# Kernel optimization log

Measured on AMD Instinct MI355X. Metric: run time of the kernel, lower is better.

Reference implementation:

```python
import jax, jax.numpy as jnp
import numpy as np

N_NODES = 50000
N_EDGES = 800000
D_IN = 128
HID = 128
N_CLS = 5
BN_EPS = 1e-5


def setup_inputs() -> dict:
    key = jax.random.key(0)
    ks = jax.random.split(key, 8)

    def lin(k, fan_in, shape):
        return (jax.random.normal(k, shape, jnp.float32) / np.sqrt(fan_in)).astype(jnp.float32)

    inp = {
        'x': jax.random.normal(ks[0], (N_NODES, D_IN), jnp.float32),
        'edge_index': jax.random.randint(ks[1], (2, N_EDGES), 0, N_NODES, dtype=jnp.int64),
        'W0': lin(ks[2], D_IN, (D_IN, HID)), 'b0': jnp.zeros((HID,), jnp.float32),
        'g0': jnp.ones((HID,), jnp.float32), 'be0': jnp.zeros((HID,), jnp.float32),
        'W1': lin(ks[3], HID, (HID, HID)), 'b1': jnp.zeros((HID,), jnp.float32),
        'g1': jnp.ones((HID,), jnp.float32), 'be1': jnp.zeros((HID,), jnp.float32),
        'W2': lin(ks[4], HID, (HID, HID)), 'b2': jnp.zeros((HID,), jnp.float32),
        'g2': jnp.ones((HID,), jnp.float32), 'be2': jnp.zeros((HID,), jnp.float32),
        'cW1': lin(ks[5], HID, (HID, HID // 2)), 'cb1': jnp.zeros((HID // 2,), jnp.float32),
        'cW2': lin(ks[6], HID // 2, (HID // 2, N_CLS)), 'cb2': jnp.zeros((N_CLS,), jnp.float32),
    }
    return inp


def _gcn_conv(x, src, dst, W, b):
    # H = D~^{-1/2} (A+I) D~^{-1/2} X W + b  (Kipf & Welling / PyG GCNConv)
    h = x @ W                                           # [N, out]
    deg = jnp.zeros((N_NODES,), h.dtype).at[dst].add(1.0) + 1.0  # degree incl. self-loop
    dinv = jax.lax.rsqrt(deg)                           # D~^{-1/2}
    norm = dinv[src] * dinv[dst]                        # [E]
    agg = jnp.zeros_like(h).at[dst].add(h[src] * norm[:, None])
    agg = agg + h * (dinv * dinv)[:, None]              # self-loop term
    return agg + b


def _batchnorm(x, gamma, beta):
    # training-mode BatchNorm1d over the node dimension
    mean = x.mean(axis=0)
    var = x.var(axis=0)
    return gamma * (x - mean) * jax.lax.rsqrt(var + BN_EPS) + beta


def reference(x, edge_index, W0, b0, g0, be0, W1, b1, g1, be1, W2, b2, g2, be2,
              cW1, cb1, cW2, cb2):
    src, dst = edge_index[0], edge_index[1]
    for W, b, g, be in ((W0, b0, g0, be0), (W1, b1, g1, be1), (W2, b2, g2, be2)):
        x = _gcn_conv(x, src, dst, W, b)
        x = _batchnorm(x, g, be)
        x = jax.nn.relu(x)
        # dropout: identity (eval / deterministic reference)
    pooled = x.mean(axis=0, keepdims=True)              # [1, HID]
    h = jax.nn.relu(pooled @ cW1 + cb1)
    return h @ cW2 + cb2                                # [1, N_CLS]
```

## Files before the change

### kernel.cpp

```cpp
#include <hip/hip_runtime.h>
#include <hip/hip_fp16.h>
#include <cstdint>
#include <cstddef>

#define D 128
#define NAGG 2048
#define SCAN_BLOCKS 256
#define FILL_PASSES 8
#define EPT 4

using f16x4 = __attribute__((ext_vector_type(4))) _Float16;
using f32x4 = __attribute__((ext_vector_type(4))) float;

__device__ __forceinline__ int swz(int row, int byte) {
  return row * 256 + (((byte)&0xF0) ^ ((row & 7) << 4)) + ((byte)&0x0F);
}


__global__ void count_kernel(const int* __restrict__ ei, int* __restrict__ counts, int E) {
  for (int e = blockIdx.x * blockDim.x + threadIdx.x; e < E; e += gridDim.x * blockDim.x) {
    int d = ei[(size_t)E + e];
    atomicAdd(&counts[d], 1);
  }
}

__global__ __launch_bounds__(256) void scan1_kernel(const int* __restrict__ counts,
                                                    int* __restrict__ blocksums, int N) {
  __shared__ int red[256];
  const int b = blockIdx.x, t = threadIdx.x;
  const int chunk = (N + SCAN_BLOCKS - 1) / SCAN_BLOCKS;
  const int lo = b * chunk, hi = min(lo + chunk, N);
  int s = 0;
  for (int i = lo + t; i < hi; i += 256) s += counts[i];
  red[t] = s;
  __syncthreads();
  for (int off = 128; off > 0; off >>= 1) {
    if (t < off) red[t] += red[t + off];
    __syncthreads();
  }
  if (t == 0) blocksums[b] = red[0];
}

__global__ __launch_bounds__(256) void scan2_kernel(int* __restrict__ blocksums) {
  __shared__ int part[256];
  const int t = threadIdx.x;
  part[t] = blocksums[t];
  __syncthreads();
  for (int off = 1; off < 256; off <<= 1) {
    int v = part[t];
    int u = (t >= off) ? part[t - off] : 0;
    __syncthreads();
    part[t] = v + u;
    __syncthreads();
  }
  blocksums[t] = (t == 0) ? 0 : part[t - 1];
}

__global__ __launch_bounds__(256) void scan3_kernel(const int* __restrict__ counts,
                                                    const int* __restrict__ blocksums,
                                                    int* __restrict__ row_ptr,
                                                    int* __restrict__ cursor,
                                                    float* __restrict__ dinv, int N) {
  __shared__ int tsum[256];
  const int b = blockIdx.x, t = threadIdx.x;
  const int chunk = (N + SCAN_BLOCKS - 1) / SCAN_BLOCKS;
  const int lo = b * chunk, hi = min(lo + chunk, N);
  const int tchunk = (chunk + 255) >> 8;
  const int tlo = lo + t * tchunk, thi = min(tlo + tchunk, hi);
  int s = 0;
  for (int i = tlo; i < thi; i++) s += counts[i];
  tsum[t] = s;
  __syncthreads();
  for (int off = 1; off < 256; off <<= 1) {
    int v = tsum[t];
    int u = (t >= off) ? tsum[t - off] : 0;
    __syncthreads();
    tsum[t] = v + u;
    __syncthreads();
  }
  int run = blocksums[b] + ((t == 0) ? 0 : tsum[t - 1]);
  for (int i = tlo; i < thi; i++) {
    int c = counts[i];
    row_ptr[i] = run; cursor[i] = run; run += c;
    dinv[i] = rsqrtf((float)c + 1.0f);
  }
  if (b == SCAN_BLOCKS - 1 && t == 255) row_ptr[N] = blocksums[b] + tsum[255];
}


__global__ __launch_bounds__(256) void fill_kernel(const int* __restrict__ ei,
                                                   int* __restrict__ cursor,
                                                   int* __restrict__ col, int E, int npp) {
  const int base = (blockIdx.x * 256 + threadIdx.x) * EPT;
  int src[EPT], dst[EPT];
#pragma unroll
  for (int j = 0; j < EPT; j++) {
    int e = base + j;
    if (e < E) { src[j] = ei[e]; dst[j] = ei[(size_t)E + e]; }
    else       { src[j] = 0;     dst[j] = -1; }
  }
  for (int p = 0; p < FILL_PASSES; p++) {
    const int lo = p * npp, hi = lo + npp;
#pragma unroll
    for (int j = 0; j < EPT; j++) {
      if (dst[j] >= lo && dst[j] < hi)
        col[atomicAdd(&cursor[dst[j]], 1)] = src[j];
    }
    __syncthreads();
  }
}


__global__ void wconv_kernel(const float* __restrict__ W0, const float* __restrict__ W1,
                             const float* __restrict__ W2, __half* __restrict__ Wt) {
  int i = blockIdx.x * 256 + threadIdx.x;
  if (i >= 3 * 128 * 128) return;
  int L = i >> 14, r = i & 16383;
  int col = r >> 7, k = r & 127;
  const float* W = (L == 0) ? W0 : (L == 1) ? W1 : W2;
  Wt[i] = __float2half(W[k * 128 + col]);
}


template <typename T>
__global__ __launch_bounds__(256, 2) void gemm_mfma_kernel(
    const T* __restrict__ A, const __half* __restrict__ Wt,
    const float* __restrict__ scale, const float* __restrict__ shift,
    const float* __restrict__ dinv, __half* __restrict__ out, int M) {
  __shared__ __align__(16) char asb[128 * 256];
  __shared__ __align__(16) char bsb[128 * 256];
  const int tid = threadIdx.x;
  const int bm = blockIdx.x * 128;

  if constexpr (sizeof(T) == 4) {
    for (int i = 0; i < 16; i++) {
      int g = tid + i * 256;
      int row = g >> 5;
      int c4 = (g & 31) << 2;
      int gr = bm + row;
      float4 v = make_float4(0.f, 0.f, 0.f, 0.f);
      if (gr < M) v = *(const float4*)(A + (size_t)gr * D + c4);
      union { float2 f2; __half h[4]; } u;
      u.h[0] = __float2half(v.x); u.h[1] = __float2half(v.y);
      u.h[2] = __float2half(v.z); u.h[3] = __float2half(v.w);
      *(float2*)(asb + swz(row, c4 * 2)) = u.f2;
    }
  } else {
    for (int i = 0; i < 8; i++) {
      int g = tid + i * 256;
      int row = g >> 4;
      int c8 = (g & 15) << 3;
      int gr = bm + row;
      union { float4 f4; __half h[8]; } u;
      if (gr < M) {
        u.f4 = *(const float4*)((const __half*)A + (size_t)gr * D + c8);
#pragma unroll
        for (int j = 0; j < 8; j++) {
          float sc = scale[c8 + j], sf = shift[c8 + j];
          u.h[j] = __float2half(fmaxf(fmaf(__half2float(u.h[j]), sc, sf), 0.f));
        }
      } else {
        u.f4 = make_float4(0.f, 0.f, 0.f, 0.f);
      }
      *(float4*)(asb + swz(row, c8 * 2)) = u.f4;
    }
  }
  for (int i = 0; i < 8; i++) {
    int g = tid + i * 256;
    int row = g >> 4;
    int sl = (g & 15) << 4;
    *(float4*)(bsb + swz(row, sl)) = *(const float4*)((const char*)Wt + (size_t)g * 16);
  }
  __syncthreads();

  const int lane = tid & 63;
  const int w = tid >> 6;
  const int l15 = lane & 15;
  const int khalf = lane >> 4;

  f32x4 acc[2][8];
#pragma unroll
  for (int m = 0; m < 2; m++)
#pragma unroll
    for (int n = 0; n < 8; n++) acc[m][n] = (f32x4){0.f, 0.f, 0.f, 0.f};

#pragma unroll
  for (int ks = 0; ks < 8; ks++) {
    int kbyte = ks * 32 + khalf * 8;
    f16x4 a0 = *(const f16x4*)(asb + swz(w * 32 + l15, kbyte));
    f16x4 a1 = *(const f16x4*)(asb + swz(w * 32 + 16 + l15, kbyte));
#pragma unroll
    for (int n = 0; n < 8; n++) {
      f16x4 b = *(const f16x4*)(bsb + swz(n * 16 + l15, kbyte));
      acc[0][n] = __builtin_amdgcn_mfma_f32_16x16x16f16(a0, b, acc[0][n], 0, 0, 0);
      acc[1][n] = __builtin_amdgcn_mfma_f32_16x16x16f16(a1, b, acc[1][n], 0, 0, 0);
    }
  }

#pragma unroll
  for (int m = 0; m < 2; m++) {
    int base_r = bm + w * 32 + m * 16 + khalf * 4;
    float dv[4];
#pragma unroll
    for (int j = 0; j < 4; j++) dv[j] = (base_r + j < M) ? dinv[base_r + j] : 0.f;
#pragma unroll
    for (int n = 0; n < 8; n++) {
      int colg = n * 16 + l15;
#pragma unroll
      for (int j = 0; j < 4; j++) {
        int r = base_r + j;
        if (r < M) out[(size_t)r * D + colg] = __float2half(acc[m][n][j] * dv[j]);
      }
    }
  }
}


__global__ __launch_bounds__(256) void agg_kernel(
    const __half* __restrict__ hp, const int* __restrict__ row_ptr, const int* __restrict__ col,
    const float* __restrict__ dinv, const float* __restrict__ bias,
    __half* __restrict__ y, float* __restrict__ pstats, int M) {
  const int tid = threadIdx.x;
  const int wave = tid >> 6;
  const int lane = tid & 63;
  const float bx = bias[lane * 2];
  const float by = bias[lane * 2 + 1];
  float sx = 0.f, sy = 0.f, qx = 0.f, qy = 0.f;

  for (int n = blockIdx.x * 4 + wave; n < M; n += gridDim.x * 4) {
    const int beg = row_ptr[n];
    const int end = row_ptr[n + 1];
    const float dn = dinv[n];
    float2 self = __half22float2(*(const __half2*)(hp + (size_t)n * D + lane * 2));
    float ax = self.x, ay = self.y;
#pragma unroll 4
    for (int e = beg; e < end; e++) {
      int s = col[e];
      float2 hv = __half22float2(*(const __half2*)(hp + (size_t)s * D + lane * 2));
      ax += hv.x; ay += hv.y;
    }
    ax = fmaf(ax, dn, bx);
    ay = fmaf(ay, dn, by);
    *(__half2*)(y + (size_t)n * D + lane * 2) = __floats2half2_rn(ax, ay);
    sx += ax; sy += ay;
    qx = fmaf(ax, ax, qx); qy = fmaf(ay, ay, qy);
  }

  __shared__ float ps[4][128];
  ps[wave][lane * 2] = sx; ps[wave][lane * 2 + 1] = sy;
  __syncthreads();
  if (tid < 128) {
    float s = ps[0][tid] + ps[1][tid] + ps[2][tid] + ps[3][tid];
    pstats[(size_t)blockIdx.x * 256 + tid] = s;
  }
  __syncthreads();
  ps[wave][lane * 2] = qx; ps[wave][lane * 2 + 1] = qy;
  __syncthreads();
  if (tid < 128) {
    float s = ps[0][tid] + ps[1][tid] + ps[2][tid] + ps[3][tid];
    pstats[(size_t)blockIdx.x * 256 + 128 + tid] = s;
  }
}


__global__ void bnred_kernel(const float* __restrict__ pstats, const float* __restrict__ g,
                             const float* __restrict__ be, float* __restrict__ scale,
                             float* __restrict__ shift, float invN) {
  const int c = blockIdx.x;
  const int tid = threadIdx.x;
  float s = 0.f, q = 0.f;
  for (int b = tid; b < NAGG; b += 256) {
    s += pstats[(size_t)b * 256 + c];
    q += pstats[(size_t)b * 256 + 128 + c];
  }
  __shared__ float rs[256], rq[256];
  rs[tid] = s; rq[tid] = q;
  __syncthreads();
  for (int off = 128; off > 0; off >>= 1) {
    if (tid < off) { rs[tid] += rs[tid + off]; rq[tid] += rq[tid + off]; }
    __syncthreads();
  }
  if (tid == 0) {
    float mean = rs[0] * invN;
    float var = rq[0] * invN - mean * mean;
    float sc = g[c] * rsqrtf(var + 1e-5f);
    scale[c] = sc;
    shift[c] = be[c] - mean * sc;
  }
}


__global__ __launch_bounds__(256) void pool_kernel(
    const __half* __restrict__ y, const float* __restrict__ scale, const float* __restrict__ shift,
    float* __restrict__ ppool, int M) {
  const int tid = threadIdx.x;
  const int wave = tid >> 6;
  const int lane = tid & 63;
  const float scx = scale[lane * 2], scy = scale[lane * 2 + 1];
  const float shx = shift[lane * 2], shy = shift[lane * 2 + 1];
  float sx = 0.f, sy = 0.f;
  for (int n = blockIdx.x * 4 + wave; n < M; n += gridDim.x * 4) {
    float2 v = __half22float2(*(const __half2*)(y + (size_t)n * D + lane * 2));
    sx += fmaxf(fmaf(v.x, scx, shx), 0.f);
    sy += fmaxf(fmaf(v.y, scy, shy), 0.f);
  }
  __shared__ float ps[4][128];
  ps[wave][lane * 2] = sx; ps[wave][lane * 2 + 1] = sy;
  __syncthreads();
  if (tid < 128) {
    float s = ps[0][tid] + ps[1][tid] + ps[2][tid] + ps[3][tid];
    ppool[(size_t)blockIdx.x * 128 + tid] = s;
  }
}

__global__ void poolred_kernel(const float* __restrict__ ppool, float* __restrict__ pooled, float invN) {
  const int c = blockIdx.x;
  const int tid = threadIdx.x;
  float s = 0.f;
  for (int b = tid; b < NAGG; b += 256) s += ppool[(size_t)b * 128 + c];
  __shared__ float rs[256];
  rs[tid] = s;
  __syncthreads();
  for (int off = 128; off > 0; off >>= 1) {
    if (tid < off) rs[tid] += rs[tid + off];
    __syncthreads();
  }
  if (tid == 0) pooled[c] = rs[0] * invN;
}


__global__ void mlp_kernel(const float* __restrict__ pooled,
                           const float* __restrict__ cW1, const float* __restrict__ cb1,
                           const float* __restrict__ cW2, const float* __restrict__ cb2,
                           float* __restrict__ outp) {
  __shared__ float pl[128];
  __shared__ float h1[64];
  const int tid = threadIdx.x;
  if (tid < 128) pl[tid] = pooled[tid];
  __syncthreads();
  if (tid < 64) {
    float s = cb1[tid];
    for (int k = 0; k < 128; k++) s = fmaf(pl[k], cW1[(size_t)k * 64 + tid], s);
    h1[tid] = fmaxf(s, 0.f);
  }
  __syncthreads();
  if (tid < 5) {
    float s = cb2[tid];
    for (int k = 0; k < 64; k++) s = fmaf(h1[k], cW2[(size_t)k * 5 + tid], s);
    outp[tid] = s;
  }
}


extern "C" void kernel_launch(void* const* d_in, const int* in_sizes, int n_in,
                              void* d_out, int out_size, void* d_ws, size_t ws_size,
                              hipStream_t stream) {
  const float* x = (const float*)d_in[0];
  const int* ei = (const int*)d_in[1];
  const float* Wm[3] = {(const float*)d_in[2], (const float*)d_in[6], (const float*)d_in[10]};
  const float* bb[3] = {(const float*)d_in[3], (const float*)d_in[7], (const float*)d_in[11]};
  const float* gg[3] = {(const float*)d_in[4], (const float*)d_in[8], (const float*)d_in[12]};
  const float* be[3] = {(const float*)d_in[5], (const float*)d_in[9], (const float*)d_in[13]};
  const float* cW1 = (const float*)d_in[14];
  const float* cb1 = (const float*)d_in[15];
  const float* cW2 = (const float*)d_in[16];
  const float* cb2 = (const float*)d_in[17];
  float* outp = (float*)d_out;

  const int N = in_sizes[0] / D;
  const int E = in_sizes[1] / 2;
  const int npp = (N + FILL_PASSES - 1) / FILL_PASSES;

  char* wsp = (char*)d_ws;
  size_t off = 0;
  auto alloc = [&](size_t bytes) -> char* {
    char* p = wsp + off;
    off += (bytes + 255) & ~(size_t)255;
    return p;
  };
  int* counts   = (int*)alloc((size_t)N * 4);
  float* dinv   = (float*)alloc((size_t)N * 4);
  int* row_ptr  = (int*)alloc((size_t)(N + 1) * 4);
  int* cursor   = (int*)alloc((size_t)N * 4);
  int* col      = (int*)alloc((size_t)E * 4);
  __half* h     = (__half*)alloc((size_t)N * D * 2);
  __half* y     = (__half*)alloc((size_t)N * D * 2);
  __half* Wt    = (__half*)alloc((size_t)3 * 128 * 128 * 2);
  float* pstats = (float*)alloc((size_t)NAGG * 256 * 4);
  float* ppool  = (float*)alloc((size_t)NAGG * 128 * 4);
  float* sc     = (float*)alloc(3 * 128 * 4);
  float* sh     = (float*)alloc(3 * 128 * 4);
  float* pooled = (float*)alloc(128 * 4);
  int* blocksums= (int*)alloc(SCAN_BLOCKS * 4);
  (void)ws_size; (void)n_in; (void)out_size;

  hipMemsetAsync(counts, 0, (size_t)N * 4, stream);
  wconv_kernel<<<192, 256, 0, stream>>>(Wm[0], Wm[1], Wm[2], Wt);
  count_kernel<<<2048, 256, 0, stream>>>(ei, counts, E);
  scan1_kernel<<<SCAN_BLOCKS, 256, 0, stream>>>(counts, blocksums, N);
  scan2_kernel<<<1, 256, 0, stream>>>(blocksums);
  scan3_kernel<<<SCAN_BLOCKS, 256, 0, stream>>>(counts, blocksums, row_ptr, cursor, dinv, N);
  {
    const int fthreads = (E + EPT - 1) / EPT;
    const int fblocks = (fthreads + 255) / 256;
    fill_kernel<<<fblocks, 256, 0, stream>>>(ei, cursor, col, E, npp);
  }

  const int gblocks = (N + 127) / 128;
  const float invN = 1.0f / (float)N;
  for (int L = 0; L < 3; L++) {
    const float* scl = (L == 0) ? nullptr : sc + (size_t)(L - 1) * 128;
    const float* shf = (L == 0) ? nullptr : sh + (size_t)(L - 1) * 128;
    if (L == 0)
      gemm_mfma_kernel<float><<<gblocks, 256, 0, stream>>>(x, Wt, scl, shf, dinv, h, N);
    else
      gemm_mfma_kernel<__half><<<gblocks, 256, 0, stream>>>(y, Wt + (size_t)L * 16384, scl, shf, dinv, h, N);
    agg_kernel<<<NAGG, 256, 0, stream>>>(h, row_ptr, col, dinv, bb[L], y, pstats, N);
    bnred_kernel<<<128, 256, 0, stream>>>(pstats, gg[L], be[L], sc + (size_t)L * 128,
                                          sh + (size_t)L * 128, invN);
  }
  pool_kernel<<<NAGG, 256, 0, stream>>>(y, sc + 256, sh + 256, ppool, N);
  poolred_kernel<<<128, 256, 0, stream>>>(ppool, pooled, invN);
  mlp_kernel<<<1, 128, 0, stream>>>(pooled, cW1, cb1, cW2, cb2, outp);
}
```

Baseline: 433.7 us.

## Rewrite GEMM to load MFMA fragments directly from global memory without LDS

```diff
diff --git a/kernel.cpp b/kernel.cpp
--- a/kernel.cpp
+++ b/kernel.cpp
@@ -11,10 +11,6 @@
 
 using f16x4 = __attribute__((ext_vector_type(4))) _Float16;
 using f32x4 = __attribute__((ext_vector_type(4))) float;
-
-__device__ __forceinline__ int swz(int row, int byte) {
-  return row * 256 + (((byte)&0xF0) ^ ((row & 7) << 4)) + ((byte)&0x0F);
-}
 
 
 __global__ void count_kernel(const int* __restrict__ ei, int* __restrict__ counts, int E) {
@@ -123,94 +119,66 @@
 
 
 template <typename T>
-__global__ __launch_bounds__(256, 2) void gemm_mfma_kernel(
+__global__ __launch_bounds__(256) void gemm_mfma_kernel(
     const T* __restrict__ A, const __half* __restrict__ Wt,
     const float* __restrict__ scale, const float* __restrict__ shift,
     const float* __restrict__ dinv, __half* __restrict__ out, int M) {
-  __shared__ __align__(16) char asb[128 * 256];
-  __shared__ __align__(16) char bsb[128 * 256];
-  const int tid = threadIdx.x;
-  const int bm = blockIdx.x * 128;
-
-  if constexpr (sizeof(T) == 4) {
-    for (int i = 0; i < 16; i++) {
-      int g = tid + i * 256;
-      int row = g >> 5;
-      int c4 = (g & 31) << 2;
-      int gr = bm + row;
-      float4 v = make_float4(0.f, 0.f, 0.f, 0.f);
-      if (gr < M) v = *(const float4*)(A + (size_t)gr * D + c4);
-      union { float2 f2; __half h[4]; } u;
-      u.h[0] = __float2half(v.x); u.h[1] = __float2half(v.y);
-      u.h[2] = __float2half(v.z); u.h[3] = __float2half(v.w);
-      *(float2*)(asb + swz(row, c4 * 2)) = u.f2;
-    }
-  } else {
-    for (int i = 0; i < 8; i++) {
-      int g = tid + i * 256;
-      int row = g >> 4;
-      int c8 = (g & 15) << 3;
-      int gr = bm + row;
-      union { float4 f4; __half h[8]; } u;
-      if (gr < M) {
-        u.f4 = *(const float4*)((const __half*)A + (size_t)gr * D + c8);
-#pragma unroll
-        for (int j = 0; j < 8; j++) {
-          float sc = scale[c8 + j], sf = shift[c8 + j];
-          u.h[j] = __float2half(fmaxf(fmaf(__half2float(u.h[j]), sc, sf), 0.f));
-        }
-      } else {
-        u.f4 = make_float4(0.f, 0.f, 0.f, 0.f);
-      }
-      *(float4*)(asb + swz(row, c8 * 2)) = u.f4;
-    }
-  }
-  for (int i = 0; i < 8; i++) {
-    int g = tid + i * 256;
-    int row = g >> 4;
-    int sl = (g & 15) << 4;
-    *(float4*)(bsb + swz(row, sl)) = *(const float4*)((const char*)Wt + (size_t)g * 16);
-  }
-  __syncthreads();
-
+  const int tid = threadIdx.x;
+  const int w = tid >> 6;
   const int lane = tid & 63;
-  const int w = tid >> 6;
   const int l15 = lane & 15;
   const int khalf = lane >> 4;
-
-  f32x4 acc[2][8];
-#pragma unroll
-  for (int m = 0; m < 2; m++)
-#pragma unroll
-    for (int n = 0; n < 8; n++) acc[m][n] = (f32x4){0.f, 0.f, 0.f, 0.f};
+  const int bm = blockIdx.x * 32;
+  const int r0 = bm + (w >> 1) * 16 + l15;
+  const int ch = (w & 1) * 64;
+  const bool rv = (r0 < M);
+
+  f32x4 acc[4];
+#pragma unroll
+  for (int n = 0; n < 4; n++) acc[n] = (f32x4){0.f, 0.f, 0.f, 0.f};
 
 #pragma unroll
   for (int ks = 0; ks < 8; ks++) {
-    int kbyte = ks * 32 + khalf * 8;
-    f16x4 a0 = *(const f16x4*)(asb + swz(w * 32 + l15, kbyte));
-    f16x4 a1 = *(const f16x4*)(asb + swz(w * 32 + 16 + l15, kbyte));
-#pragma unroll
-    for (int n = 0; n < 8; n++) {
-      f16x4 b = *(const f16x4*)(bsb + swz(n * 16 + l15, kbyte));
-      acc[0][n] = __builtin_amdgcn_mfma_f32_16x16x16f16(a0, b, acc[0][n], 0, 0, 0);
-      acc[1][n] = __builtin_amdgcn_mfma_f32_16x16x16f16(a1, b, acc[1][n], 0, 0, 0);
-    }
-  }
-
-#pragma unroll
-  for (int m = 0; m < 2; m++) {
-    int base_r = bm + w * 32 + m * 16 + khalf * 4;
-    float dv[4];
-#pragma unroll
-    for (int j = 0; j < 4; j++) dv[j] = (base_r + j < M) ? dinv[base_r + j] : 0.f;
-#pragma unroll
-    for (int n = 0; n < 8; n++) {
-      int colg = n * 16 + l15;
-#pragma unroll
-      for (int j = 0; j < 4; j++) {
-        int r = base_r + j;
-        if (r < M) out[(size_t)r * D + colg] = __float2half(acc[m][n][j] * dv[j]);
+    const int k0 = ks * 16 + khalf * 4;
+    union { f16x4 v; __half h[4]; } ua;
+    if constexpr (sizeof(T) == 4) {
+      float4 av = rv ? *(const float4*)(A + (size_t)r0 * D + k0)
+                     : make_float4(0.f, 0.f, 0.f, 0.f);
+      ua.h[0] = __float2half(av.x); ua.h[1] = __float2half(av.y);
+      ua.h[2] = __float2half(av.z); ua.h[3] = __float2half(av.w);
+    } else {
+      if (rv) {
+        union { f16x4 v; __half h[4]; } raw;
+        raw.v = *(const f16x4*)((const __half*)A + (size_t)r0 * D + k0);
+        float4 sc4 = *(const float4*)(scale + k0);
+        float4 sh4 = *(const float4*)(shift + k0);
+        ua.h[0] = __float2half(fmaxf(fmaf(__half2float(raw.h[0]), sc4.x, sh4.x), 0.f));
+        ua.h[1] = __float2half(fmaxf(fmaf(__half2float(raw.h[1]), sc4.y, sh4.y), 0.f));
+        ua.h[2] = __float2half(fmaxf(fmaf(__half2float(raw.h[2]), sc4.z, sh4.z), 0.f));
+        ua.h[3] = __float2half(fmaxf(fmaf(__half2float(raw.h[3]), sc4.w, sh4.w), 0.f));
+      } else {
+        ua.v = (f16x4){0, 0, 0, 0};
       }
+    }
+#pragma unroll
+    for (int n = 0; n < 4; n++) {
+      const int col = ch + n * 16 + l15;
+      f16x4 b = *(const f16x4*)(Wt + (size_t)col * D + k0);
+      acc[n] = __builtin_amdgcn_mfma_f32_16x16x16f16(ua.v, b, acc[n], 0, 0, 0);
+    }
+  }
+
+  const int base_r = bm + (w >> 1) * 16 + khalf * 4;
+  float dv[4];
+#pragma unroll
+  for (int j = 0; j < 4; j++) dv[j] = (base_r + j < M) ? dinv[base_r + j] : 0.f;
+#pragma unroll
+  for (int n = 0; n < 4; n++) {
+    const int c = ch + n * 16 + l15;
+#pragma unroll
+    for (int j = 0; j < 4; j++) {
+      const int r = base_r + j;
+      if (r < M) out[(size_t)r * D + c] = __float2half(acc[n][j] * dv[j]);
     }
   }
 }
@@ -406,7 +374,7 @@
     fill_kernel<<<fblocks, 256, 0, stream>>>(ei, cursor, col, E, npp);
   }
 
-  const int gblocks = (N + 127) / 128;
+  const int gblocks = (N + 31) / 32;
   const float invN = 1.0f / (float)N;
   for (int L = 0; L < 3; L++) {
     const float* scl = (L == 0) ? nullptr : sc + (size_t)(L - 1) * 128;
```

Measured after the change: 452.0 us. 4.2% more time.
